# Kernel tuning notes

Measured on AMD Instinct MI355X. Metric: run time of the kernel, lower is better.

## Reference

```python
import jax, jax.numpy as jnp
import numpy as np

N_INP = 10
N_REC = 200
ALPHA = 0.1          # dt / tau = 0.01 / 0.1
NOISE_STD = 0.01
W_REC_SCALE = 0.5
W_INP_SCALE = 0.1
BATCH = 256
T = 1000


def setup_inputs() -> dict:
    key = jax.random.key(0)
    kx, kwi, kwr = jax.random.split(key, 3)
    x = jax.random.normal(kx, (BATCH, T, N_INP), dtype=jnp.float32)
    h0 = jnp.zeros((BATCH, N_REC), dtype=jnp.float32)
    W_inp = (W_INP_SCALE / np.sqrt(N_INP)) * jax.random.normal(kwi, (N_REC, N_INP), dtype=jnp.float32)
    W_rec = (W_REC_SCALE / np.sqrt(N_REC)) * jax.random.normal(kwr, (N_REC, N_REC), dtype=jnp.float32)
    b_rec = jnp.zeros((N_REC,), dtype=jnp.float32)
    return {"x": x, "h0": h0, "W_inp": W_inp, "W_rec": W_rec, "b_rec": b_rec}


def reference(x, h0, W_inp, W_rec, b_rec):
    """Euler-discretized rate RNN: h' = h + alpha*(-h + tanh(W_rec h + W_inp x + b) + noise).
    Returns states: [batch, time, n_rec]."""
    B, Tlen, _ = x.shape
    # Precompute input drive for all timesteps in one GEMM: [B,T,n_rec]
    inp_term = jnp.einsum('bti,ri->btr', x, W_inp) + b_rec
    # Per-step noise, deterministic key (mirrors torch.randn_like each step)
    noise_key = jax.random.key(42)
    eta = NOISE_STD * jax.random.normal(noise_key, (Tlen, B, W_rec.shape[0]), dtype=x.dtype)

    def step(h, xs):
        inp_t, eta_t = xs
        preact = h @ W_rec.T + inp_t          # [B, n_rec]
        rate = jnp.tanh(preact)
        h_next = h + ALPHA * (-h + rate + eta_t)
        return h_next, h_next

    _, states = jax.lax.scan(step, h0, (jnp.swapaxes(inp_term, 0, 1), eta))
    return jnp.swapaxes(states, 0, 1)  # [B, T, n_rec]
```

## Files before the change

kernel.cpp:

```cpp
#include <hip/hip_runtime.h>
#include <cstdint>
#include <cstddef>

#define TSTEPS 1000
#define NB     256
#define NR     200
#define NI     10
#define ALPHA_F     0.1f
#define NOISE_STD_F 0.01f
#define ETA_STRIDE  (NB * NR)
#define ETA_FLOATS  ((size_t)TSTEPS * NB * NR)

__device__ __forceinline__ uint32_t rotl32(uint32_t v, uint32_t d) {
  return (v << d) | (v >> (32u - d));
}

__device__ __forceinline__ uint32_t threefry_bits(uint32_t c1) {
  const uint32_t ks0 = 0u;
  const uint32_t ks1 = 42u;
  const uint32_t ks2 = 0x1BD11BDAu ^ ks0 ^ ks1;
  uint32_t x0 = ks0;
  uint32_t x1 = c1 + ks1;
#define TFR(r) { x0 += x1; x1 = rotl32(x1, (r)); x1 ^= x0; }
  TFR(13) TFR(15) TFR(26) TFR(6)   x0 += ks1; x1 += ks2 + 1u;
// ... 40 lines not shown
  const float lo = -0.99999994f;
  float u = fmaf(f, 2.0f, lo);
  u = fmaxf(lo, u);
  return 1.41421356f * erfinv_f32(u);
}

__device__ __forceinline__ float tanh_fast(float y) {
  float ay = fabsf(y);
  float t  = __expf(-2.0f * ay);
  float r  = (1.0f - t) * __frcp_rn(1.0f + t);
  return copysignf(r, y);
}

__device__ __forceinline__ void wg_barrier_lds() {
  asm volatile("s_waitcnt lgkmcnt(0)\n\ts_barrier" ::: "memory");
}

__launch_bounds__(256)
__global__ void noise_fill(float* __restrict__ ws) {
  const int64_t nq = (int64_t)ETA_FLOATS / 4;
  const int64_t stride = (int64_t)gridDim.x * blockDim.x;
  for (int64_t i = (int64_t)blockIdx.x * blockDim.x + threadIdx.x;
       i < nq; i += stride) {
    uint32_t base = (uint32_t)(i * 4);
    float4 v;
    v.x = NOISE_STD_F * jax_normal(base + 0u);
    v.y = NOISE_STD_F * jax_normal(base + 1u);
    v.z = NOISE_STD_F * jax_normal(base + 2u);
    v.w = NOISE_STD_F * jax_normal(base + 3u);
    ((float4*)ws)[i] = v;
  }
}

template <int CUR, bool PF, bool PRE>
__device__ __forceinline__ void rnn_step(
    int t, int tid, bool mac_active,
    const float (&w)[4][20], const float (&winp)[NI], float brec_r,
    float& h_reg, float*& obp, float& xnA, float& xnB,
    float4& enA, float4& enB,
    const float* __restrict__ xb, const float* __restrict__ etab,
    uint32_t nb_b,
    const float* __restrict__ hp, float* __restrict__ part_wp,
    float* __restrict__ sh_h, float* __restrict__ sh_part,
    float (*__restrict__ sh_x)[16], float (*__restrict__ sh_eta)[NR]) {
  constexpr int NXT = CUR ^ 1;

  if (mac_active) {
    float a0 = 0.0f, a1 = 0.0f, a2 = 0.0f, a3 = 0.0f;
#pragma unroll
    for (int q = 0; q < 5; ++q) {
      float4 hv = *(const float4*)(hp + 4 * q);
      a0 = fmaf(w[0][4 * q + 0], hv.x, a0);
      a1 = fmaf(w[1][4 * q + 0], hv.x, a1);
      a2 = fmaf(w[2][4 * q + 0], hv.x, a2);
      a3 = fmaf(w[3][4 * q + 0], hv.x, a3);
      a0 = fmaf(w[0][4 * q + 1], hv.y, a0);
      a1 = fmaf(w[1][4 * q + 1], hv.y, a1);
      a2 = fmaf(w[2][4 * q + 1], hv.y, a2);
      a3 = fmaf(w[3][4 * q + 1], hv.y, a3);
      a0 = fmaf(w[0][4 * q + 2], hv.z, a0);
      a1 = fmaf(w[1][4 * q + 2], hv.z, a1);
      a2 = fmaf(w[2][4 * q + 2], hv.z, a2);
      a3 = fmaf(w[3][4 * q + 2], hv.z, a3);
      a0 = fmaf(w[0][4 * q + 3], hv.w, a0);
      a1 = fmaf(w[1][4 * q + 3], hv.w, a1);
      a2 = fmaf(w[2][4 * q + 3], hv.w, a2);
      a3 = fmaf(w[3][4 * q + 3], hv.w, a3);
    }
    *(float4*)part_wp = make_float4(a0, a1, a2, a3);
  }
  wg_barrier_lds();

  if (tid < NR) {
    float y = brec_r;
#pragma unroll
    for (int q = 0; q < 10; ++q) y += sh_part[q * NR + tid];
    float4 xv0 = *(const float4*)(&sh_x[CUR][0]);
    float4 xv1 = *(const float4*)(&sh_x[CUR][4]);
    float2 xv2 = *(const float2*)(&sh_x[CUR][8]);
    y = fmaf(winp[0], xv0.x, y);
    y = fmaf(winp[1], xv0.y, y);
    y = fmaf(winp[2], xv0.z, y);
    y = fmaf(winp[3], xv0.w, y);
    y = fmaf(winp[4], xv1.x, y);
    y = fmaf(winp[5], xv1.y, y);
    y = fmaf(winp[6], xv1.z, y);
    y = fmaf(winp[7], xv1.w, y);
    y = fmaf(winp[8], xv2.x, y);
    y = fmaf(winp[9], xv2.y, y);
    float rate = tanh_fast(y);
    float eta  = sh_eta[CUR][tid];
    float hn = h_reg + ALPHA_F * (((-h_reg) + rate) + eta);
    h_reg = hn;
    sh_h[tid] = hn;
    *obp = hn;
    obp += NR;
  } else if (PRE ? (tid >= 256 && tid < 256 + NR / 4)
                 : ((tid >= 256 && tid < 448) || (tid < 208))) {
    if (PF) {
      if constexpr (PRE) {
        int j = tid - 256;
        *(float4*)(&sh_eta[NXT][4 * j]) = (CUR == 0) ? enA : enB;
        int tf = t + 3;
        if (tf > TSTEPS - 1) tf = TSTEPS - 1;
        float4 e = *(const float4*)(etab + (size_t)tf * ETA_STRIDE + 4 * j);
        if (CUR == 0) enA = e; else enB = e;
      } else {
        int n = (tid >= 256) ? (tid - 256) : (tid - 8);
        uint32_t idx = (uint32_t)(t + 1) * (uint32_t)(NB * NR) + nb_b + (uint32_t)n;
        sh_eta[NXT][n] = NOISE_STD_F * jax_normal(idx);
      }
    }
  } else if (tid >= 448 && tid < 448 + NI) {
    if (PF) {
      int j = tid - 448;
      sh_x[NXT][j] = (CUR == 0) ? xnA : xnB;
      int tf = t + 3;
      if (tf > TSTEPS - 1) tf = TSTEPS - 1;
      float xl = xb[tf * NI + j];
      if (CUR == 0) xnA = xl; else xnB = xl;
    }
  }
  wg_barrier_lds();
}

template <bool PRE>
__global__ __launch_bounds__(512, 2)
void rnn_persistent(const float* __restrict__ x,
                    const float* __restrict__ h0,
                    const float* __restrict__ Winp,
                    const float* __restrict__ Wrec,
                    const float* __restrict__ brec,
                    const float* __restrict__ eta_ws,
                    float* __restrict__ out) {
  const int b   = blockIdx.x;
  const int tid = threadIdx.x;

  __shared__ float sh_h[NR];
  __shared__ float sh_part[10 * NR];
  __shared__ float sh_x[2][16];
  __shared__ float sh_eta[2][NR];

  const int  k_th = tid / 50;
  const int  r_th = tid % 50;
  const bool mac_active = (tid < 500);

  float w[4][20];
  if (mac_active) {
#pragma unroll
    for (int j = 0; j < 4; ++j) {
      const float* wr = Wrec + (size_t)(4 * r_th + j) * NR + 20 * k_th;
#pragma unroll
      for (int q = 0; q < 5; ++q) {
        float4 v = *(const float4*)(wr + 4 * q);
        w[j][4 * q + 0] = v.x; w[j][4 * q + 1] = v.y;
        w[j][4 * q + 2] = v.z; w[j][4 * q + 3] = v.w;
      }
    }
  }

  float winp[NI];
  float brec_r = 0.0f;
  float h_reg  = 0.0f;
  float* obp   = nullptr;

  const float* xb   = x + (size_t)b * TSTEPS * NI;
  const float* etab = PRE ? (eta_ws + (size_t)b * NR) : nullptr;
  float* ob         = out + (size_t)b * TSTEPS * NR;

  if (tid < NR) {
#pragma unroll
    for (int i = 0; i < NI; ++i) winp[i] = Winp[tid * NI + i];
    brec_r = brec[tid];
    h_reg  = h0[(size_t)b * NR + tid];
    sh_h[tid] = h_reg;
    obp = ob + tid;
  }

  const uint32_t nb_b = (uint32_t)b * (uint32_t)NR;
  float  xnA = 0.0f, xnB = 0.0f;
  float4 enA = make_float4(0.f, 0.f, 0.f, 0.f);
  float4 enB = make_float4(0.f, 0.f, 0.f, 0.f);

  if constexpr (PRE) {
    if (tid >= 256 && tid < 256 + NR / 4) {
      int j = tid - 256;
      *(float4*)(&sh_eta[0][4 * j]) = *(const float4*)(etab + 4 * j);
      enA = *(const float4*)(etab + (size_t)1 * ETA_STRIDE + 4 * j);
      enB = *(const float4*)(etab + (size_t)2 * ETA_STRIDE + 4 * j);
    }
  } else {
    if ((tid >= 256 && tid < 448) || (tid >= 200 && tid < 208)) {
      int n = (tid >= 256) ? (tid - 256) : (tid - 8);
      sh_eta[0][n] = NOISE_STD_F * jax_normal(nb_b + (uint32_t)n);
    }
  }
  if (tid >= 448 && tid < 448 + NI) {
    int j = tid - 448;
    sh_x[0][j] = xb[j];
    xnA = xb[NI + j];
    xnB = xb[2 * NI + j];
  }
  __syncthreads();

  const float* hp      = sh_h + 20 * k_th;
  float*       part_wp = sh_part + k_th * NR + 4 * r_th;

  for (int t = 0; t < TSTEPS - 2; t += 2) {
    rnn_step<0, true, PRE>(t,     tid, mac_active, w, winp, brec_r, h_reg, obp,
                           xnA, xnB, enA, enB, xb, etab, nb_b, hp, part_wp,
                           sh_h, sh_part, sh_x, sh_eta);
    rnn_step<1, true, PRE>(t + 1, tid, mac_active, w, winp, brec_r, h_reg, obp,
                           xnA, xnB, enA, enB, xb, etab, nb_b, hp, part_wp,
                           sh_h, sh_part, sh_x, sh_eta);
  }
  rnn_step<0, true,  PRE>(TSTEPS - 2, tid, mac_active, w, winp, brec_r, h_reg, obp,
                          xnA, xnB, enA, enB, xb, etab, nb_b, hp, part_wp,
                          sh_h, sh_part, sh_x, sh_eta);
  rnn_step<1, false, PRE>(TSTEPS - 1, tid, mac_active, w, winp, brec_r, h_reg, obp,
                          xnA, xnB, enA, enB, xb, etab, nb_b, hp, part_wp,
                          sh_h, sh_part, sh_x, sh_eta);
}

extern "C" void kernel_launch(void* const* d_in, const int* in_sizes, int n_in,
                              void* d_out, int out_size, void* d_ws, size_t ws_size,
                              hipStream_t stream) {
  const float* x    = (const float*)d_in[0];
  const float* h0   = (const float*)d_in[1];
  const float* Winp = (const float*)d_in[2];
  const float* Wrec = (const float*)d_in[3];
  const float* brec = (const float*)d_in[4];
  float* out = (float*)d_out;
  (void)in_sizes; (void)n_in; (void)out_size;

  const size_t eta_bytes = ETA_FLOATS * sizeof(float);
  if (d_ws != nullptr && ws_size >= eta_bytes) {
    noise_fill<<<dim3(4096), dim3(256), 0, stream>>>((float*)d_ws);
    rnn_persistent<true><<<dim3(NB), dim3(512), 0, stream>>>(
        x, h0, Winp, Wrec, brec, (const float*)d_ws, out);
  } else {
    rnn_persistent<false><<<dim3(NB), dim3(512), 0, stream>>>(
        x, h0, Winp, Wrec, brec, nullptr, out);
  }
}
```

Before: 885.7 us.

## Pack two batch rows per workgroup and ping-pong matvec with update phases

```diff
diff --git a/kernel.cpp b/kernel.cpp
--- a/kernel.cpp
+++ b/kernel.cpp
@@ -96,20 +96,13 @@
   }
 }
 
-template <int CUR, bool PF, bool PRE>
-__device__ __forceinline__ void rnn_step(
-    int t, int tid, bool mac_active,
-    const float (&w)[4][20], const float (&winp)[NI], float brec_r,
-    float& h_reg, float*& obp, float& xnA, float& xnB,
-    float4& enA, float4& enB,
-    const float* __restrict__ xb, const float* __restrict__ etab,
-    uint32_t nb_b,
-    const float* __restrict__ hp, float* __restrict__ part_wp,
-    float* __restrict__ sh_h, float* __restrict__ sh_part,
-    float (*__restrict__ sh_x)[16], float (*__restrict__ sh_eta)[NR]) {
-  constexpr int NXT = CUR ^ 1;
-
-  if (mac_active) {
+
+__device__ __forceinline__ void do_mac(
+    bool mac_active, const float (&w)[4][40],
+    const float* __restrict__ hp,
+    float* __restrict__ p0, float* __restrict__ p1) {
+  if (!mac_active) return;
+  {
     float a0 = 0.0f, a1 = 0.0f, a2 = 0.0f, a3 = 0.0f;
 #pragma unroll
     for (int q = 0; q < 5; ++q) {
@@ -131,10 +124,236 @@
       a2 = fmaf(w[2][4 * q + 3], hv.w, a2);
       a3 = fmaf(w[3][4 * q + 3], hv.w, a3);
     }
+    *(float4*)p0 = make_float4(a0, a1, a2, a3);
+  }
+  {
+    float a0 = 0.0f, a1 = 0.0f, a2 = 0.0f, a3 = 0.0f;
+#pragma unroll
+    for (int q = 0; q < 5; ++q) {
+      float4 hv = *(const float4*)(hp + 20 + 4 * q);
+      a0 = fmaf(w[0][20 + 4 * q + 0], hv.x, a0);
+      a1 = fmaf(w[1][20 + 4 * q + 0], hv.x, a1);
+      a2 = fmaf(w[2][20 + 4 * q + 0], hv.x, a2);
+      a3 = fmaf(w[3][20 + 4 * q + 0], hv.x, a3);
+      a0 = fmaf(w[0][20 + 4 * q + 1], hv.y, a0);
+      a1 = fmaf(w[1][20 + 4 * q + 1], hv.y, a1);
+      a2 = fmaf(w[2][20 + 4 * q + 1], hv.y, a2);
+      a3 = fmaf(w[3][20 + 4 * q + 1], hv.y, a3);
+      a0 = fmaf(w[0][20 + 4 * q + 2], hv.z, a0);
+      a1 = fmaf(w[1][20 + 4 * q + 2], hv.z, a1);
+      a2 = fmaf(w[2][20 + 4 * q + 2], hv.z, a2);
+      a3 = fmaf(w[3][20 + 4 * q + 2], hv.z, a3);
+      a0 = fmaf(w[0][20 + 4 * q + 3], hv.w, a0);
+      a1 = fmaf(w[1][20 + 4 * q + 3], hv.w, a1);
+      a2 = fmaf(w[2][20 + 4 * q + 3], hv.w, a2);
+      a3 = fmaf(w[3][20 + 4 * q + 3], hv.w, a3);
+    }
+    *(float4*)p1 = make_float4(a0, a1, a2, a3);
+  }
+}
+
+template <int CUR, bool PF>
+__device__ __forceinline__ void do_upd(
+    int t, int lt,
+    const float (&winp)[NI], float brec_r, float& h_reg, float*& obp,
+    float4& enA, float4& enB, float2& xnA, float2& xnB,
+    const float* __restrict__ xb, const float* __restrict__ etab,
+    float* __restrict__ g_h, const float* __restrict__ g_part,
+    float (*__restrict__ g_x)[16], float (*__restrict__ g_eta)[NR]) {
+  constexpr int NXT = CUR ^ 1;
+  if (lt < NR) {
+    float y = brec_r;
+#pragma unroll
+    for (int q = 0; q < 10; ++q) y += g_part[q * NR + lt];
+    float4 xv0 = *(const float4*)(&g_x[CUR][0]);
+    float4 xv1 = *(const float4*)(&g_x[CUR][4]);
+    float2 xv2 = *(const float2*)(&g_x[CUR][8]);
+    y = fmaf(winp[0], xv0.x, y);
+    y = fmaf(winp[1], xv0.y, y);
+    y = fmaf(winp[2], xv0.z, y);
+    y = fmaf(winp[3], xv0.w, y);
+    y = fmaf(winp[4], xv1.x, y);
+    y = fmaf(winp[5], xv1.y, y);
+    y = fmaf(winp[6], xv1.z, y);
+    y = fmaf(winp[7], xv1.w, y);
+    y = fmaf(winp[8], xv2.x, y);
+    y = fmaf(winp[9], xv2.y, y);
+    float rate = tanh_fast(y);
+    float eta  = g_eta[CUR][lt];
+    float hn = h_reg + ALPHA_F * (((-h_reg) + rate) + eta);
+    h_reg = hn;
+    g_h[lt] = hn;
+    *obp = hn;
+    obp += NR;
+  } else if (lt < 250) {
+    if (PF) {
+      int j = lt - 200;
+      *(float4*)(&g_eta[NXT][4 * j]) = (CUR == 0) ? enA : enB;
+      int tf = t + 3;
+      if (tf > TSTEPS - 1) tf = TSTEPS - 1;
+      float4 e = *(const float4*)(etab + (size_t)tf * ETA_STRIDE + 4 * j);
+      if (CUR == 0) enA = e; else enB = e;
+    }
+  } else if (lt < 255) {
+    if (PF) {
+      int j = lt - 250;
+      *(float2*)(&g_x[NXT][2 * j]) = (CUR == 0) ? xnA : xnB;
+      int tf = t + 3;
+      if (tf > TSTEPS - 1) tf = TSTEPS - 1;
+      float2 xl = *(const float2*)(xb + tf * NI + 2 * j);
+      if (CUR == 0) xnA = xl; else xnB = xl;
+    }
+  }
+}
+
+__launch_bounds__(512, 2)
+__global__ void rnn_dual(const float* __restrict__ x,
+                         const float* __restrict__ h0,
+                         const float* __restrict__ Winp,
+                         const float* __restrict__ Wrec,
+                         const float* __restrict__ brec,
+                         const float* __restrict__ eta_ws,
+                         float* __restrict__ out) {
+  const int wg  = blockIdx.x;
+  const int tid = threadIdx.x;
+  const int grp = tid >> 8;
+  const int lt  = tid & 255;
+  const int b   = 2 * wg + grp;
+
+  __shared__ float sh_h[2][NR];
+  __shared__ float sh_part[2][10 * NR];
+  __shared__ float sh_x[2][2][16];
+  __shared__ float sh_eta[2][2][NR];
+
+  float* g_h    = sh_h[grp];
+  float* g_part = sh_part[grp];
+  float (*g_x)[16]  = sh_x[grp];
+  float (*g_eta)[NR] = sh_eta[grp];
+
+  const int  k_th = lt / 50;
+  const int  r_th = lt % 50;
+  const bool mac_active = (lt < 250);
+
+  float w[4][40];
+  if (mac_active) {
+#pragma unroll
+    for (int j = 0; j < 4; ++j) {
+      const float* wr = Wrec + (size_t)(4 * r_th + j) * NR + 40 * k_th;
+#pragma unroll
+      for (int q = 0; q < 10; ++q) {
+        float4 v = *(const float4*)(wr + 4 * q);
+        w[j][4 * q + 0] = v.x; w[j][4 * q + 1] = v.y;
+        w[j][4 * q + 2] = v.z; w[j][4 * q + 3] = v.w;
+      }
+    }
+  }
+
+  float winp[NI];
+  float brec_r = 0.0f;
+  float h_reg  = 0.0f;
+  float* obp   = nullptr;
+
+  const float* xb   = x + (size_t)b * TSTEPS * NI;
+  const float* etab = eta_ws + (size_t)b * NR;
+  float* ob         = out + (size_t)b * TSTEPS * NR;
+
+  if (lt < NR) {
+#pragma unroll
+    for (int i = 0; i < NI; ++i) winp[i] = Winp[lt * NI + i];
+    brec_r = brec[lt];
+    h_reg  = h0[(size_t)b * NR + lt];
+    g_h[lt] = h_reg;
+    obp = ob + lt;
+  }
+
+  float4 enA = make_float4(0.f, 0.f, 0.f, 0.f);
+  float4 enB = make_float4(0.f, 0.f, 0.f, 0.f);
+  float2 xnA = make_float2(0.f, 0.f);
+  float2 xnB = make_float2(0.f, 0.f);
+
+  if (lt >= 200 && lt < 250) {
+    int j = lt - 200;
+    *(float4*)(&g_eta[0][4 * j]) = *(const float4*)(etab + 4 * j);
+    enA = *(const float4*)(etab + (size_t)1 * ETA_STRIDE + 4 * j);
+    enB = *(const float4*)(etab + (size_t)2 * ETA_STRIDE + 4 * j);
+  } else if (lt >= 250 && lt < 255) {
+    int j = lt - 250;
+    *(float2*)(&g_x[0][2 * j]) = *(const float2*)(xb + 2 * j);
+    xnA = *(const float2*)(xb + NI + 2 * j);
+    xnB = *(const float2*)(xb + 2 * NI + 2 * j);
+  }
+  __syncthreads();
+
+  const float* hp = g_h + 40 * k_th;
+  float* p0 = g_part + (size_t)(2 * k_th) * NR + 4 * r_th;
+  float* p1 = g_part + (size_t)(2 * k_th + 1) * NR + 4 * r_th;
+
+  if (grp == 0) do_mac(mac_active, w, hp, p0, p1);
+  wg_barrier_lds();
+
+#define SLOT_B(I, C, P)                                                     \
+  if (grp == 0) do_upd<C, P>((I), lt, winp, brec_r, h_reg, obp, enA, enB,   \
+                             xnA, xnB, xb, etab, g_h, g_part, g_x, g_eta);  \
+  else          do_mac(mac_active, w, hp, p0, p1);                          \
+  wg_barrier_lds();
+#define SLOT_A(I, C, P)                                                     \
+  if (grp == 0) do_mac(mac_active, w, hp, p0, p1);                          \
+  else          do_upd<C, P>((I)-1, lt, winp, brec_r, h_reg, obp, enA, enB, \
+                             xnA, xnB, xb, etab, g_h, g_part, g_x, g_eta);  \
+  wg_barrier_lds();
+
+  for (int i = 0; i < TSTEPS - 2; i += 2) {
+    SLOT_B(i,     0, true)
+    SLOT_A(i + 1, 0, true)
+    SLOT_B(i + 1, 1, true)
+    SLOT_A(i + 2, 1, true)
+  }
+  SLOT_B(TSTEPS - 2, 0, true)
+  SLOT_A(TSTEPS - 1, 0, true)
+  SLOT_B(TSTEPS - 1, 1, false)
+  if (grp == 1) {
+    do_upd<1, false>(TSTEPS - 1, lt, winp, brec_r, h_reg, obp, enA, enB,
+                     xnA, xnB, xb, etab, g_h, g_part, g_x, g_eta);
+  }
+#undef SLOT_A
+#undef SLOT_B
+}
+
+template <int CUR, bool PF>
+__device__ __forceinline__ void fb_step(
+    int t, int tid, bool mac_active,
+    const float (&w)[4][20], const float (&winp)[NI], float brec_r,
+    float& h_reg, float*& obp, float& xnA, float& xnB,
+    const float* __restrict__ xb, uint32_t nb_b,
+    const float* __restrict__ hp, float* __restrict__ part_wp,
+    float* __restrict__ sh_h, float* __restrict__ sh_part,
+    float (*__restrict__ sh_x)[16], float (*__restrict__ sh_eta)[NR]) {
+  constexpr int NXT = CUR ^ 1;
+  if (mac_active) {
+    float a0 = 0.0f, a1 = 0.0f, a2 = 0.0f, a3 = 0.0f;
+#pragma unroll
+    for (int q = 0; q < 5; ++q) {
+      float4 hv = *(const float4*)(hp + 4 * q);
+      a0 = fmaf(w[0][4 * q + 0], hv.x, a0);
+      a1 = fmaf(w[1][4 * q + 0], hv.x, a1);
+      a2 = fmaf(w[2][4 * q + 0], hv.x, a2);
+      a3 = fmaf(w[3][4 * q + 0], hv.x, a3);
+      a0 = fmaf(w[0][4 * q + 1], hv.y, a0);
+      a1 = fmaf(w[1][4 * q + 1], hv.y, a1);
+      a2 = fmaf(w[2][4 * q + 1], hv.y, a2);
+      a3 = fmaf(w[3][4 * q + 1], hv.y, a3);
+      a0 = fmaf(w[0][4 * q + 2], hv.z, a0);
+      a1 = fmaf(w[1][4 * q + 2], hv.z, a1);
+      a2 = fmaf(w[2][4 * q + 2], hv.z, a2);
+      a3 = fmaf(w[3][4 * q + 2], hv.z, a3);
+      a0 = fmaf(w[0][4 * q + 3], hv.w, a0);
+      a1 = fmaf(w[1][4 * q + 3], hv.w, a1);
+      a2 = fmaf(w[2][4 * q + 3], hv.w, a2);
+      a3 = fmaf(w[3][4 * q + 3], hv.w, a3);
+    }
     *(float4*)part_wp = make_float4(a0, a1, a2, a3);
   }
   wg_barrier_lds();
-
   if (tid < NR) {
     float y = brec_r;
 #pragma unroll
@@ -159,21 +378,11 @@
     sh_h[tid] = hn;
     *obp = hn;
     obp += NR;
-  } else if (PRE ? (tid >= 256 && tid < 256 + NR / 4)
-                 : ((tid >= 256 && tid < 448) || (tid < 208))) {
+  } else if ((tid >= 256 && tid < 448) || (tid < 208)) {
     if (PF) {
-      if constexpr (PRE) {
-        int j = tid - 256;
-        *(float4*)(&sh_eta[NXT][4 * j]) = (CUR == 0) ? enA : enB;
-        int tf = t + 3;
-        if (tf > TSTEPS - 1) tf = TSTEPS - 1;
-        float4 e = *(const float4*)(etab + (size_t)tf * ETA_STRIDE + 4 * j);
-        if (CUR == 0) enA = e; else enB = e;
-      } else {
-        int n = (tid >= 256) ? (tid - 256) : (tid - 8);
-        uint32_t idx = (uint32_t)(t + 1) * (uint32_t)(NB * NR) + nb_b + (uint32_t)n;
-        sh_eta[NXT][n] = NOISE_STD_F * jax_normal(idx);
-      }
+      int n = (tid >= 256) ? (tid - 256) : (tid - 8);
+      uint32_t idx = (uint32_t)(t + 1) * (uint32_t)(NB * NR) + nb_b + (uint32_t)n;
+      sh_eta[NXT][n] = NOISE_STD_F * jax_normal(idx);
     }
   } else if (tid >= 448 && tid < 448 + NI) {
     if (PF) {
@@ -188,27 +397,22 @@
   wg_barrier_lds();
 }
 
-template <bool PRE>
 __global__ __launch_bounds__(512, 2)
-void rnn_persistent(const float* __restrict__ x,
-                    const float* __restrict__ h0,
-                    const float* __restrict__ Winp,
-                    const float* __restrict__ Wrec,
-                    const float* __restrict__ brec,
-                    const float* __restrict__ eta_ws,
-                    float* __restrict__ out) {
+void rnn_fallback(const float* __restrict__ x,
+                  const float* __restrict__ h0,
+                  const float* __restrict__ Winp,
+                  const float* __restrict__ Wrec,
+                  const float* __restrict__ brec,
+                  float* __restrict__ out) {
   const int b   = blockIdx.x;
   const int tid = threadIdx.x;
-
   __shared__ float sh_h[NR];
   __shared__ float sh_part[10 * NR];
   __shared__ float sh_x[2][16];
   __shared__ float sh_eta[2][NR];
-
   const int  k_th = tid / 50;
   const int  r_th = tid % 50;
   const bool mac_active = (tid < 500);
-
   float w[4][20];
   if (mac_active) {
 #pragma unroll
@@ -222,16 +426,11 @@
       }
     }
   }
-
   float winp[NI];
-  float brec_r = 0.0f;
-  float h_reg  = 0.0f;
-  float* obp   = nullptr;
-
-  const float* xb   = x + (size_t)b * TSTEPS * NI;
-  const float* etab = PRE ? (eta_ws + (size_t)b * NR) : nullptr;
-  float* ob         = out + (size_t)b * TSTEPS * NR;
-
+  float brec_r = 0.0f, h_reg = 0.0f;
+  float* obp = nullptr;
+  const float* xb = x + (size_t)b * TSTEPS * NI;
+  float* ob       = out + (size_t)b * TSTEPS * NR;
   if (tid < NR) {
 #pragma unroll
     for (int i = 0; i < NI; ++i) winp[i] = Winp[tid * NI + i];
@@ -240,24 +439,11 @@
     sh_h[tid] = h_reg;
     obp = ob + tid;
   }
-
   const uint32_t nb_b = (uint32_t)b * (uint32_t)NR;
-  float  xnA = 0.0f, xnB = 0.0f;
-  float4 enA = make_float4(0.f, 0.f, 0.f, 0.f);
-  float4 enB = make_float4(0.f, 0.f, 0.f, 0.f);
-
-  if constexpr (PRE) {
-    if (tid >= 256 && tid < 256 + NR / 4) {
-      int j = tid - 256;
-      *(float4*)(&sh_eta[0][4 * j]) = *(const float4*)(etab + 4 * j);
-      enA = *(const float4*)(etab + (size_t)1 * ETA_STRIDE + 4 * j);
-      enB = *(const float4*)(etab + (size_t)2 * ETA_STRIDE + 4 * j);
-    }
-  } else {
-    if ((tid >= 256 && tid < 448) || (tid >= 200 && tid < 208)) {
-      int n = (tid >= 256) ? (tid - 256) : (tid - 8);
-      sh_eta[0][n] = NOISE_STD_F * jax_normal(nb_b + (uint32_t)n);
-    }
+  float xnA = 0.0f, xnB = 0.0f;
+  if ((tid >= 256 && tid < 448) || (tid >= 200 && tid < 208)) {
+    int n = (tid >= 256) ? (tid - 256) : (tid - 8);
+    sh_eta[0][n] = NOISE_STD_F * jax_normal(nb_b + (uint32_t)n);
   }
   if (tid >= 448 && tid < 448 + NI) {
     int j = tid - 448;
@@ -266,24 +452,18 @@
     xnB = xb[2 * NI + j];
   }
   __syncthreads();
-
   const float* hp      = sh_h + 20 * k_th;
   float*       part_wp = sh_part + k_th * NR + 4 * r_th;
-
   for (int t = 0; t < TSTEPS - 2; t += 2) {
-    rnn_step<0, true, PRE>(t,     tid, mac_active, w, winp, brec_r, h_reg, obp,
-                           xnA, xnB, enA, enB, xb, etab, nb_b, hp, part_wp,
-                           sh_h, sh_part, sh_x, sh_eta);
-    rnn_step<1, true, PRE>(t + 1, tid, mac_active, w, winp, brec_r, h_reg, obp,
-                           xnA, xnB, enA, enB, xb, etab, nb_b, hp, part_wp,
-                           sh_h, sh_part, sh_x, sh_eta);
-  }
-  rnn_step<0, true,  PRE>(TSTEPS - 2, tid, mac_active, w, winp, brec_r, h_reg, obp,
-                          xnA, xnB, enA, enB, xb, etab, nb_b, hp, part_wp,
-                          sh_h, sh_part, sh_x, sh_eta);
-  rnn_step<1, false, PRE>(TSTEPS - 1, tid, mac_active, w, winp, brec_r, h_reg, obp,
-                          xnA, xnB, enA, enB, xb, etab, nb_b, hp, part_wp,
-                          sh_h, sh_part, sh_x, sh_eta);
+    fb_step<0, true>(t,     tid, mac_active, w, winp, brec_r, h_reg, obp,
+                     xnA, xnB, xb, nb_b, hp, part_wp, sh_h, sh_part, sh_x, sh_eta);
+    fb_step<1, true>(t + 1, tid, mac_active, w, winp, brec_r, h_reg, obp,
+                     xnA, xnB, xb, nb_b, hp, part_wp, sh_h, sh_part, sh_x, sh_eta);
+  }
+  fb_step<0, true >(TSTEPS - 2, tid, mac_active, w, winp, brec_r, h_reg, obp,
+                    xnA, xnB, xb, nb_b, hp, part_wp, sh_h, sh_part, sh_x, sh_eta);
+  fb_step<1, false>(TSTEPS - 1, tid, mac_active, w, winp, brec_r, h_reg, obp,
+                    xnA, xnB, xb, nb_b, hp, part_wp, sh_h, sh_part, sh_x, sh_eta);
 }
 
 extern "C" void kernel_launch(void* const* d_in, const int* in_sizes, int n_in,
@@ -300,10 +480,10 @@
   const size_t eta_bytes = ETA_FLOATS * sizeof(float);
   if (d_ws != nullptr && ws_size >= eta_bytes) {
     noise_fill<<<dim3(4096), dim3(256), 0, stream>>>((float*)d_ws);
-    rnn_persistent<true><<<dim3(NB), dim3(512), 0, stream>>>(
+    rnn_dual<<<dim3(NB / 2), dim3(512), 0, stream>>>(
         x, h0, Winp, Wrec, brec, (const float*)d_ws, out);
   } else {
-    rnn_persistent<false><<<dim3(NB), dim3(512), 0, stream>>>(
-        x, h0, Winp, Wrec, brec, nullptr, out);
-  }
-}
+    rnn_fallback<<<dim3(NB), dim3(512), 0, stream>>>(
+        x, h0, Winp, Wrec, brec, out);
+  }
+}
```

New measurement: 1.759 ms. 98.6% more time.

## Keep full W_rec rows in registers, one thread per output row

Applied to the files above, without the earlier changes.

```diff
diff --git a/kernel.cpp b/kernel.cpp
--- a/kernel.cpp
+++ b/kernel.cpp
@@ -96,19 +96,186 @@
   }
 }
 
-template <int CUR, bool PF, bool PRE>
-__device__ __forceinline__ void rnn_step(
+
+#define DECLW(q) \
+  float W_##q##_0 = 0.f, W_##q##_1 = 0.f, W_##q##_2 = 0.f, W_##q##_3 = 0.f, \
+        W_##q##_4 = 0.f, W_##q##_5 = 0.f, W_##q##_6 = 0.f, W_##q##_7 = 0.f, \
+        W_##q##_8 = 0.f, W_##q##_9 = 0.f, W_##q##_10 = 0.f, W_##q##_11 = 0.f,\
+        W_##q##_12 = 0.f, W_##q##_13 = 0.f, W_##q##_14 = 0.f,               \
+        W_##q##_15 = 0.f, W_##q##_16 = 0.f, W_##q##_17 = 0.f,               \
+        W_##q##_18 = 0.f, W_##q##_19 = 0.f;
+
+#define LOADW(q) {                                                          \
+  const float* wp_ = wr + 20 * (q);                                         \
+  float4 a_  = *(const float4*)(wp_);                                       \
+  float4 b_  = *(const float4*)(wp_ + 4);                                   \
+  float4 c_  = *(const float4*)(wp_ + 8);                                   \
+  float4 d_  = *(const float4*)(wp_ + 12);                                  \
+  float4 e4_ = *(const float4*)(wp_ + 16);                                  \
+  W_##q##_0  = a_.x;  W_##q##_1  = a_.y;  W_##q##_2  = a_.z;                \
+  W_##q##_3  = a_.w;  W_##q##_4  = b_.x;  W_##q##_5  = b_.y;                \
+  W_##q##_6  = b_.z;  W_##q##_7  = b_.w;  W_##q##_8  = c_.x;                \
+  W_##q##_9  = c_.y;  W_##q##_10 = c_.z;  W_##q##_11 = c_.w;                \
+  W_##q##_12 = d_.x;  W_##q##_13 = d_.y;  W_##q##_14 = d_.z;                \
+  W_##q##_15 = d_.w;  W_##q##_16 = e4_.x; W_##q##_17 = e4_.y;               \
+  W_##q##_18 = e4_.z; W_##q##_19 = e4_.w; }
+
+#define FMAC(q) {                                                           \
+  const float* hq_ = hb + 20 * (q);                                         \
+  float4 a_  = *(const float4*)(hq_);                                       \
+  float4 b_  = *(const float4*)(hq_ + 4);                                   \
+  float4 c_  = *(const float4*)(hq_ + 8);                                   \
+  float4 d_  = *(const float4*)(hq_ + 12);                                  \
+  float4 e4_ = *(const float4*)(hq_ + 16);                                  \
+  float p_ = 0.0f;                                                          \
+  p_ = fmaf(W_##q##_0,  a_.x,  p_);                                         \
+  p_ = fmaf(W_##q##_1,  a_.y,  p_);                                         \
+  p_ = fmaf(W_##q##_2,  a_.z,  p_);                                         \
+  p_ = fmaf(W_##q##_3,  a_.w,  p_);                                         \
+  p_ = fmaf(W_##q##_4,  b_.x,  p_);                                         \
+  p_ = fmaf(W_##q##_5,  b_.y,  p_);                                         \
+  p_ = fmaf(W_##q##_6,  b_.z,  p_);                                         \
+  p_ = fmaf(W_##q##_7,  b_.w,  p_);                                         \
+  p_ = fmaf(W_##q##_8,  c_.x,  p_);                                         \
+  p_ = fmaf(W_##q##_9,  c_.y,  p_);                                         \
+  p_ = fmaf(W_##q##_10, c_.z,  p_);                                         \
+  p_ = fmaf(W_##q##_11, c_.w,  p_);                                         \
+  p_ = fmaf(W_##q##_12, d_.x,  p_);                                         \
+  p_ = fmaf(W_##q##_13, d_.y,  p_);                                         \
+  p_ = fmaf(W_##q##_14, d_.z,  p_);                                         \
+  p_ = fmaf(W_##q##_15, d_.w,  p_);                                         \
+  p_ = fmaf(W_##q##_16, e4_.x, p_);                                         \
+  p_ = fmaf(W_##q##_17, e4_.y, p_);                                         \
+  p_ = fmaf(W_##q##_18, e4_.z, p_);                                         \
+  p_ = fmaf(W_##q##_19, e4_.w, p_);                                         \
+  y += p_; }
+
+#define STEP(CURI, TT, PF_) {                                               \
+  if (ln < 50) {                                                            \
+    const float* hb = sh_h[CURI];                                           \
+    float y = brec_r;                                                       \
+    FMAC(0) FMAC(1) FMAC(2) FMAC(3) FMAC(4)                                 \
+    FMAC(5) FMAC(6) FMAC(7) FMAC(8) FMAC(9)                                 \
+    float4 xv0 = *(const float4*)(&sh_x[CURI][0]);                          \
+    float4 xv1 = *(const float4*)(&sh_x[CURI][4]);                          \
+    float2 xv2 = *(const float2*)(&sh_x[CURI][8]);                          \
+    y = fmaf(winp0, xv0.x, y);                                              \
+    y = fmaf(winp1, xv0.y, y);                                              \
+    y = fmaf(winp2, xv0.z, y);                                              \
+    y = fmaf(winp3, xv0.w, y);                                              \
+    y = fmaf(winp4, xv1.x, y);                                              \
+    y = fmaf(winp5, xv1.y, y);                                              \
+    y = fmaf(winp6, xv1.z, y);                                              \
+    y = fmaf(winp7, xv1.w, y);                                              \
+    y = fmaf(winp8, xv2.x, y);                                              \
+    y = fmaf(winp9, xv2.y, y);                                              \
+    float rate = tanh_fast(y);                                              \
+    float eta  = sh_eta[CURI][row];                                         \
+    float hn = h_reg + ALPHA_F * (((-h_reg) + rate) + eta);                 \
+    h_reg = hn;                                                             \
+    sh_h[(CURI) ^ 1][row] = hn;                                             \
+    *obp = hn;                                                              \
+    obp += NR;                                                              \
+  } else if (elane) {                                                       \
+    if (PF_) {                                                              \
+      *(float4*)(&sh_eta[(CURI) ^ 1][4 * eidx]) =                           \
+          ((CURI) == 0) ? enA : enB;                                        \
+      int tf = (TT) + 3;                                                    \
+      if (tf > TSTEPS - 1) tf = TSTEPS - 1;                                 \
+      float4 e_ = *(const float4*)(etab + (size_t)tf * ETA_STRIDE + 4 * eidx);\
+      if ((CURI) == 0) enA = e_; else enB = e_;                             \
+    }                                                                       \
+  } else if (xlane) {                                                       \
+    if (PF_) {                                                              \
+      *(float2*)(&sh_x[(CURI) ^ 1][2 * xj]) = ((CURI) == 0) ? xnA : xnB;    \
+      int tf = (TT) + 3;                                                    \
+      if (tf > TSTEPS - 1) tf = TSTEPS - 1;                                 \
+      float2 x_ = *(const float2*)(xb + tf * NI + 2 * xj);                  \
+      if ((CURI) == 0) xnA = x_; else xnB = x_;                             \
+    }                                                                       \
+  }                                                                         \
+  wg_barrier_lds(); }
+
+__launch_bounds__(256, 1)
+__global__ void rnn_rowreg(const float* __restrict__ x,
+                           const float* __restrict__ h0,
+                           const float* __restrict__ Winp,
+                           const float* __restrict__ Wrec,
+                           const float* __restrict__ brec,
+                           const float* __restrict__ eta_ws,
+                           float* __restrict__ out) {
+  const int b   = blockIdx.x;
+  const int tid = threadIdx.x;
+  const int wv  = tid >> 6;
+  const int ln  = tid & 63;
+
+  __shared__ float sh_h[2][NR];
+  __shared__ float sh_eta[2][NR];
+  __shared__ float sh_x[2][16];
+
+  const int  row  = wv * 50 + ln;
+  const int  eidx = wv * 13 + (ln - 50);
+  const bool elane = (ln >= 50) && (ln < 63) && (eidx < 50);
+  const bool xlane = (ln == 63) || (wv == 3 && ln == 61);
+  const int  xj    = (ln == 63) ? wv : 4;
+
+  const float* xb   = x + (size_t)b * TSTEPS * NI;
+  const float* etab = eta_ws + (size_t)b * NR;
+  float* ob         = out + (size_t)b * TSTEPS * NR;
+
+  DECLW(0) DECLW(1) DECLW(2) DECLW(3) DECLW(4)
+  DECLW(5) DECLW(6) DECLW(7) DECLW(8) DECLW(9)
+  float winp0 = 0.f, winp1 = 0.f, winp2 = 0.f, winp3 = 0.f, winp4 = 0.f;
+  float winp5 = 0.f, winp6 = 0.f, winp7 = 0.f, winp8 = 0.f, winp9 = 0.f;
+  float brec_r = 0.0f;
+  float h_reg  = 0.0f;
+  float* obp   = nullptr;
+  float4 enA = make_float4(0.f, 0.f, 0.f, 0.f);
+  float4 enB = make_float4(0.f, 0.f, 0.f, 0.f);
+  float2 xnA = make_float2(0.f, 0.f);
+  float2 xnB = make_float2(0.f, 0.f);
+
+  if (ln < 50) {
+    const float* wr = Wrec + (size_t)row * NR;
+    LOADW(0) LOADW(1) LOADW(2) LOADW(3) LOADW(4)
+    LOADW(5) LOADW(6) LOADW(7) LOADW(8) LOADW(9)
+    const float* wi = Winp + (size_t)row * NI;
+    winp0 = wi[0]; winp1 = wi[1]; winp2 = wi[2]; winp3 = wi[3];
+    winp4 = wi[4]; winp5 = wi[5]; winp6 = wi[6]; winp7 = wi[7];
+    winp8 = wi[8]; winp9 = wi[9];
+    brec_r = brec[row];
+    h_reg  = h0[(size_t)b * NR + row];
+    sh_h[0][row] = h_reg;
+    obp = ob + row;
+  } else if (elane) {
+    *(float4*)(&sh_eta[0][4 * eidx]) = *(const float4*)(etab + 4 * eidx);
+    enA = *(const float4*)(etab + (size_t)1 * ETA_STRIDE + 4 * eidx);
+    enB = *(const float4*)(etab + (size_t)2 * ETA_STRIDE + 4 * eidx);
+  } else if (xlane) {
+    *(float2*)(&sh_x[0][2 * xj]) = *(const float2*)(xb + 2 * xj);
+    xnA = *(const float2*)(xb + NI + 2 * xj);
+    xnB = *(const float2*)(xb + 2 * NI + 2 * xj);
+  }
+  __syncthreads();
+
+  for (int t = 0; t < TSTEPS - 2; t += 2) {
+    STEP(0, t,     true)
+    STEP(1, t + 1, true)
+  }
+  STEP(0, TSTEPS - 2, true)
+  STEP(1, TSTEPS - 1, false)
+}
+
+template <int CUR, bool PF>
+__device__ __forceinline__ void fb_step(
     int t, int tid, bool mac_active,
     const float (&w)[4][20], const float (&winp)[NI], float brec_r,
     float& h_reg, float*& obp, float& xnA, float& xnB,
-    float4& enA, float4& enB,
-    const float* __restrict__ xb, const float* __restrict__ etab,
-    uint32_t nb_b,
+    const float* __restrict__ xb, uint32_t nb_b,
     const float* __restrict__ hp, float* __restrict__ part_wp,
     float* __restrict__ sh_h, float* __restrict__ sh_part,
     float (*__restrict__ sh_x)[16], float (*__restrict__ sh_eta)[NR]) {
   constexpr int NXT = CUR ^ 1;
-
   if (mac_active) {
     float a0 = 0.0f, a1 = 0.0f, a2 = 0.0f, a3 = 0.0f;
 #pragma unroll
@@ -134,7 +301,6 @@
     *(float4*)part_wp = make_float4(a0, a1, a2, a3);
   }
   wg_barrier_lds();
-
   if (tid < NR) {
     float y = brec_r;
 #pragma unroll
@@ -159,21 +325,11 @@
     sh_h[tid] = hn;
     *obp = hn;
     obp += NR;
-  } else if (PRE ? (tid >= 256 && tid < 256 + NR / 4)
-                 : ((tid >= 256 && tid < 448) || (tid < 208))) {
+  } else if ((tid >= 256 && tid < 448) || (tid < 208)) {
     if (PF) {
-      if constexpr (PRE) {
-        int j = tid - 256;
-        *(float4*)(&sh_eta[NXT][4 * j]) = (CUR == 0) ? enA : enB;
-        int tf = t + 3;
-        if (tf > TSTEPS - 1) tf = TSTEPS - 1;
-        float4 e = *(const float4*)(etab + (size_t)tf * ETA_STRIDE + 4 * j);
-        if (CUR == 0) enA = e; else enB = e;
-      } else {
-        int n = (tid >= 256) ? (tid - 256) : (tid - 8);
-        uint32_t idx = (uint32_t)(t + 1) * (uint32_t)(NB * NR) + nb_b + (uint32_t)n;
-        sh_eta[NXT][n] = NOISE_STD_F * jax_normal(idx);
-      }
+      int n = (tid >= 256) ? (tid - 256) : (tid - 8);
+      uint32_t idx = (uint32_t)(t + 1) * (uint32_t)(NB * NR) + nb_b + (uint32_t)n;
+      sh_eta[NXT][n] = NOISE_STD_F * jax_normal(idx);
     }
   } else if (tid >= 448 && tid < 448 + NI) {
     if (PF) {
@@ -188,27 +344,22 @@
   wg_barrier_lds();
 }
 
-template <bool PRE>
 __global__ __launch_bounds__(512, 2)
-void rnn_persistent(const float* __restrict__ x,
-                    const float* __restrict__ h0,
-                    const float* __restrict__ Winp,
-                    const float* __restrict__ Wrec,
-                    const float* __restrict__ brec,
-                    const float* __restrict__ eta_ws,
-                    float* __restrict__ out) {
+void rnn_fallback(const float* __restrict__ x,
+                  const float* __restrict__ h0,
+                  const float* __restrict__ Winp,
+                  const float* __restrict__ Wrec,
+                  const float* __restrict__ brec,
+                  float* __restrict__ out) {
   const int b   = blockIdx.x;
   const int tid = threadIdx.x;
-
   __shared__ float sh_h[NR];
   __shared__ float sh_part[10 * NR];
   __shared__ float sh_x[2][16];
   __shared__ float sh_eta[2][NR];
-
   const int  k_th = tid / 50;
   const int  r_th = tid % 50;
   const bool mac_active = (tid < 500);
-
   float w[4][20];
   if (mac_active) {
 #pragma unroll
@@ -222,16 +373,11 @@
       }
     }
   }
-
   float winp[NI];
-  float brec_r = 0.0f;
-  float h_reg  = 0.0f;
-  float* obp   = nullptr;
-
-  const float* xb   = x + (size_t)b * TSTEPS * NI;
-  const float* etab = PRE ? (eta_ws + (size_t)b * NR) : nullptr;
-  float* ob         = out + (size_t)b * TSTEPS * NR;
-
+  float brec_r = 0.0f, h_reg = 0.0f;
+  float* obp = nullptr;
+  const float* xb = x + (size_t)b * TSTEPS * NI;
+  float* ob       = out + (size_t)b * TSTEPS * NR;
   if (tid < NR) {
 #pragma unroll
     for (int i = 0; i < NI; ++i) winp[i] = Winp[tid * NI + i];
@@ -240,24 +386,11 @@
     sh_h[tid] = h_reg;
     obp = ob + tid;
   }
-
   const uint32_t nb_b = (uint32_t)b * (uint32_t)NR;
-  float  xnA = 0.0f, xnB = 0.0f;
-  float4 enA = make_float4(0.f, 0.f, 0.f, 0.f);
-  float4 enB = make_float4(0.f, 0.f, 0.f, 0.f);
-
-  if constexpr (PRE) {
-    if (tid >= 256 && tid < 256 + NR / 4) {
-      int j = tid - 256;
-      *(float4*)(&sh_eta[0][4 * j]) = *(const float4*)(etab + 4 * j);
-      enA = *(const float4*)(etab + (size_t)1 * ETA_STRIDE + 4 * j);
-      enB = *(const float4*)(etab + (size_t)2 * ETA_STRIDE + 4 * j);
-    }
-  } else {
-    if ((tid >= 256 && tid < 448) || (tid >= 200 && tid < 208)) {
-      int n = (tid >= 256) ? (tid - 256) : (tid - 8);
-      sh_eta[0][n] = NOISE_STD_F * jax_normal(nb_b + (uint32_t)n);
-    }
+  float xnA = 0.0f, xnB = 0.0f;
+  if ((tid >= 256 && tid < 448) || (tid >= 200 && tid < 208)) {
+    int n = (tid >= 256) ? (tid - 256) : (tid - 8);
+    sh_eta[0][n] = NOISE_STD_F * jax_normal(nb_b + (uint32_t)n);
   }
   if (tid >= 448 && tid < 448 + NI) {
     int j = tid - 448;
@@ -266,24 +399,18 @@
     xnB = xb[2 * NI + j];
   }
   __syncthreads();
-
   const float* hp      = sh_h + 20 * k_th;
   float*       part_wp = sh_part + k_th * NR + 4 * r_th;
-
   for (int t = 0; t < TSTEPS - 2; t += 2) {
-    rnn_step<0, true, PRE>(t,     tid, mac_active, w, winp, brec_r, h_reg, obp,
-                           xnA, xnB, enA, enB, xb, etab, nb_b, hp, part_wp,
-                           sh_h, sh_part, sh_x, sh_eta);
-    rnn_step<1, true, PRE>(t + 1, tid, mac_active, w, winp, brec_r, h_reg, obp,
-                           xnA, xnB, enA, enB, xb, etab, nb_b, hp, part_wp,
-                           sh_h, sh_part, sh_x, sh_eta);
-  }
-  rnn_step<0, true,  PRE>(TSTEPS - 2, tid, mac_active, w, winp, brec_r, h_reg, obp,
-                          xnA, xnB, enA, enB, xb, etab, nb_b, hp, part_wp,
-                          sh_h, sh_part, sh_x, sh_eta);
-  rnn_step<1, false, PRE>(TSTEPS - 1, tid, mac_active, w, winp, brec_r, h_reg, obp,
-                          xnA, xnB, enA, enB, xb, etab, nb_b, hp, part_wp,
-                          sh_h, sh_part, sh_x, sh_eta);
+    fb_step<0, true>(t,     tid, mac_active, w, winp, brec_r, h_reg, obp,
+                     xnA, xnB, xb, nb_b, hp, part_wp, sh_h, sh_part, sh_x, sh_eta);
+    fb_step<1, true>(t + 1, tid, mac_active, w, winp, brec_r, h_reg, obp,
+                     xnA, xnB, xb, nb_b, hp, part_wp, sh_h, sh_part, sh_x, sh_eta);
+  }
+  fb_step<0, true >(TSTEPS - 2, tid, mac_active, w, winp, brec_r, h_reg, obp,
+                    xnA, xnB, xb, nb_b, hp, part_wp, sh_h, sh_part, sh_x, sh_eta);
+  fb_step<1, false>(TSTEPS - 1, tid, mac_active, w, winp, brec_r, h_reg, obp,
+                    xnA, xnB, xb, nb_b, hp, part_wp, sh_h, sh_part, sh_x, sh_eta);
 }
 
 extern "C" void kernel_launch(void* const* d_in, const int* in_sizes, int n_in,
@@ -300,10 +427,10 @@
   const size_t eta_bytes = ETA_FLOATS * sizeof(float);
   if (d_ws != nullptr && ws_size >= eta_bytes) {
     noise_fill<<<dim3(4096), dim3(256), 0, stream>>>((float*)d_ws);
-    rnn_persistent<true><<<dim3(NB), dim3(512), 0, stream>>>(
+    rnn_rowreg<<<dim3(NB), dim3(256), 0, stream>>>(
         x, h0, Winp, Wrec, brec, (const float*)d_ws, out);
   } else {
-    rnn_persistent<false><<<dim3(NB), dim3(512), 0, stream>>>(
-        x, h0, Winp, Wrec, brec, nullptr, out);
-  }
-}
+    rnn_fallback<<<dim3(NB), dim3(512), 0, stream>>>(
+        x, h0, Winp, Wrec, brec, out);
+  }
+}
```

New measurement: 1.421 ms. +60.5%, slower.

## Restructure RNN step into 8-row MAC tiles with separate update waves

Applied to the files above, without the earlier changes.

```diff
diff --git a/kernel.cpp b/kernel.cpp
--- a/kernel.cpp
+++ b/kernel.cpp
@@ -96,19 +96,184 @@
   }
 }
 
-template <int CUR, bool PF, bool PRE>
-__device__ __forceinline__ void rnn_step(
+
+#define DECLW8(r) float4 W##r##_0, W##r##_1, W##r##_2, W##r##_3, W##r##_4;
+
+#define LOADW8(r) {                                                         \
+  const float* wp_ = Wrec + (size_t)(8 * r_th + (r)) * NR + 20 * k_th;      \
+  W##r##_0 = *(const float4*)(wp_);                                         \
+  W##r##_1 = *(const float4*)(wp_ + 4);                                     \
+  W##r##_2 = *(const float4*)(wp_ + 8);                                     \
+  W##r##_3 = *(const float4*)(wp_ + 12);                                    \
+  W##r##_4 = *(const float4*)(wp_ + 16); }
+
+#define ROWACC(r)                                                           \
+  float a##r = 0.0f;                                                        \
+  a##r = fmaf(W##r##_0.x, h0_.x, a##r);                                     \
+  a##r = fmaf(W##r##_0.y, h0_.y, a##r);                                     \
+  a##r = fmaf(W##r##_0.z, h0_.z, a##r);                                     \
+  a##r = fmaf(W##r##_0.w, h0_.w, a##r);                                     \
+  a##r = fmaf(W##r##_1.x, h1_.x, a##r);                                     \
+  a##r = fmaf(W##r##_1.y, h1_.y, a##r);                                     \
+  a##r = fmaf(W##r##_1.z, h1_.z, a##r);                                     \
+  a##r = fmaf(W##r##_1.w, h1_.w, a##r);                                     \
+  a##r = fmaf(W##r##_2.x, h2_.x, a##r);                                     \
+  a##r = fmaf(W##r##_2.y, h2_.y, a##r);                                     \
+  a##r = fmaf(W##r##_2.z, h2_.z, a##r);                                     \
+  a##r = fmaf(W##r##_2.w, h2_.w, a##r);                                     \
+  a##r = fmaf(W##r##_3.x, h3_.x, a##r);                                     \
+  a##r = fmaf(W##r##_3.y, h3_.y, a##r);                                     \
+  a##r = fmaf(W##r##_3.z, h3_.z, a##r);                                     \
+  a##r = fmaf(W##r##_3.w, h3_.w, a##r);                                     \
+  a##r = fmaf(W##r##_4.x, h4_.x, a##r);                                     \
+  a##r = fmaf(W##r##_4.y, h4_.y, a##r);                                     \
+  a##r = fmaf(W##r##_4.z, h4_.z, a##r);                                     \
+  a##r = fmaf(W##r##_4.w, h4_.w, a##r);
+
+#define STEP(CURI, TT) {                                                    \
+                        \
+  if (mac_active) {                                                         \
+    float4 h0_ = *(const float4*)(hb);                                      \
+    float4 h1_ = *(const float4*)(hb + 4);                                  \
+    float4 h2_ = *(const float4*)(hb + 8);                                  \
+    float4 h3_ = *(const float4*)(hb + 12);                                 \
+    float4 h4_ = *(const float4*)(hb + 16);                                 \
+    ROWACC(0) ROWACC(1) ROWACC(2) ROWACC(3)                                 \
+    ROWACC(4) ROWACC(5) ROWACC(6) ROWACC(7)                                 \
+    *(float4*)pw0 = make_float4(a0, a1, a2, a3);                            \
+    *(float4*)pw1 = make_float4(a4, a5, a6, a7);                            \
+  }                                                                         \
+  wg_barrier_lds();                                                         \
+                        \
+  if (upd_active) {                                                         \
+    float y = brec_r;                                                       \
+    y += pr[0 * 208];                                                       \
+    y += pr[1 * 208];                                                       \
+    y += pr[2 * 208];                                                       \
+    y += pr[3 * 208];                                                       \
+    y += pr[4 * 208];                                                       \
+    y += pr[5 * 208];                                                       \
+    y += pr[6 * 208];                                                       \
+    y += pr[7 * 208];                                                       \
+    y += pr[8 * 208];                                                       \
+    y += pr[9 * 208];                                                       \
+    float4 xv0 = *(const float4*)(&sh_x[CURI][0]);                          \
+    float4 xv1 = *(const float4*)(&sh_x[CURI][4]);                          \
+    float2 xv2 = *(const float2*)(&sh_x[CURI][8]);                          \
+    y = fmaf(winp[0], xv0.x, y);                                            \
+    y = fmaf(winp[1], xv0.y, y);                                            \
+    y = fmaf(winp[2], xv0.z, y);                                            \
+    y = fmaf(winp[3], xv0.w, y);                                            \
+    y = fmaf(winp[4], xv1.x, y);                                            \
+    y = fmaf(winp[5], xv1.y, y);                                            \
+    y = fmaf(winp[6], xv1.z, y);                                            \
+    y = fmaf(winp[7], xv1.w, y);                                            \
+    y = fmaf(winp[8], xv2.x, y);                                            \
+    y = fmaf(winp[9], xv2.y, y);                                            \
+    float rate = tanh_fast(y);                                              \
+    float eta  = (CURI == 0) ? etaA : etaB;                                 \
+    float hn = h_reg + ALPHA_F * (((-h_reg) + rate) + eta);                 \
+    h_reg = hn;                                                             \
+    sh_h[urow] = hn;                                                        \
+    *obp = hn;                                                              \
+    obp += NR;                                                              \
+    int tf_ = (TT) + 2;                                                     \
+    if (tf_ > TSTEPS - 1) tf_ = TSTEPS - 1;    \
+    float e_ = etab[(size_t)tf_ * ETA_STRIDE + urow];                       \
+    if (CURI == 0) etaA = e_; else etaB = e_;                               \
+  } else if (xpipe) {                                                       \
+    *(float2*)(&sh_x[(CURI) ^ 1][2 * xj]) = (CURI == 0) ? xnA : xnB;        \
+    int tf_ = (TT) + 3;                                                     \
+    if (tf_ > TSTEPS - 1) tf_ = TSTEPS - 1;                                 \
+    float2 x_ = *(const float2*)(xb + tf_ * NI + 2 * xj);                   \
+    if (CURI == 0) xnA = x_; else xnB = x_;                                 \
+  }                                                                         \
+  wg_barrier_lds(); }
+
+__launch_bounds__(512, 1)
+__global__ void rnn_r8(const float* __restrict__ x,
+                       const float* __restrict__ h0,
+                       const float* __restrict__ Winp,
+                       const float* __restrict__ Wrec,
+                       const float* __restrict__ brec,
+                       const float* __restrict__ eta_ws,
+                       float* __restrict__ out) {
+  const int b   = blockIdx.x;
+  const int tid = threadIdx.x;
+  const int wv  = tid >> 6;
+  const int ln  = tid & 63;
+
+  __shared__ float sh_h[NR];
+  __shared__ float sh_part[10 * 208];
+  __shared__ float sh_x[2][16];
+
+  const bool mac_active = (tid < 250);
+  const int  k_th = tid / 25;
+  const int  r_th = tid % 25;
+
+  const bool upd_active = (wv >= 4) && (ln < 50);
+  const int  urow = (wv - 4) * 50 + ln;
+  const bool xpipe = (wv == 4) && (ln >= 50) && (ln < 55);
+  const int  xj    = ln - 50;
+
+  const float* xb   = x + (size_t)b * TSTEPS * NI;
+  const float* etab = eta_ws + (size_t)b * NR;
+  float* ob         = out + (size_t)b * TSTEPS * NR;
+
+  DECLW8(0) DECLW8(1) DECLW8(2) DECLW8(3)
+  DECLW8(4) DECLW8(5) DECLW8(6) DECLW8(7)
+  const float* hb = nullptr;
+  float* pw0 = nullptr;
+  float* pw1 = nullptr;
+
+  float winp[NI];
+  float brec_r = 0.0f;
+  float h_reg  = 0.0f;
+  float etaA = 0.0f, etaB = 0.0f;
+  float* obp = nullptr;
+  const float* pr = nullptr;
+  float2 xnA = make_float2(0.f, 0.f);
+  float2 xnB = make_float2(0.f, 0.f);
+
+  if (mac_active) {
+    LOADW8(0) LOADW8(1) LOADW8(2) LOADW8(3)
+    LOADW8(4) LOADW8(5) LOADW8(6) LOADW8(7)
+    hb  = sh_h + 20 * k_th;
+    pw0 = sh_part + 208 * k_th + 4 * r_th;
+    pw1 = pw0 + 104;
+  } else if (upd_active) {
+#pragma unroll
+    for (int i = 0; i < NI; ++i) winp[i] = Winp[urow * NI + i];
+    brec_r = brec[urow];
+    h_reg  = h0[(size_t)b * NR + urow];
+    sh_h[urow] = h_reg;
+    obp = ob + urow;
+    pr = sh_part + 4 * (urow >> 3) + (urow & 3) + ((urow & 7) >= 4 ? 104 : 0);
+    etaA = etab[urow];
+    etaB = etab[(size_t)1 * ETA_STRIDE + urow];
+  } else if (xpipe) {
+    *(float2*)(&sh_x[0][2 * xj]) = *(const float2*)(xb + 2 * xj);
+    xnA = *(const float2*)(xb + NI + 2 * xj);
+    xnB = *(const float2*)(xb + 2 * NI + 2 * xj);
+  }
+  __syncthreads();
+
+  for (int t = 0; t < TSTEPS; t += 2) {
+    STEP(0, t)
+    STEP(1, t + 1)
+  }
+}
+
+template <int CUR, bool PF>
+__device__ __forceinline__ void fb_step(
     int t, int tid, bool mac_active,
     const float (&w)[4][20], const float (&winp)[NI], float brec_r,
     float& h_reg, float*& obp, float& xnA, float& xnB,
-    float4& enA, float4& enB,
-    const float* __restrict__ xb, const float* __restrict__ etab,
-    uint32_t nb_b,
+    const float* __restrict__ xb, uint32_t nb_b,
     const float* __restrict__ hp, float* __restrict__ part_wp,
     float* __restrict__ sh_h, float* __restrict__ sh_part,
     float (*__restrict__ sh_x)[16], float (*__restrict__ sh_eta)[NR]) {
   constexpr int NXT = CUR ^ 1;
-
   if (mac_active) {
     float a0 = 0.0f, a1 = 0.0f, a2 = 0.0f, a3 = 0.0f;
 #pragma unroll
@@ -134,7 +299,6 @@
     *(float4*)part_wp = make_float4(a0, a1, a2, a3);
   }
   wg_barrier_lds();
-
   if (tid < NR) {
     float y = brec_r;
 #pragma unroll
@@ -159,21 +323,11 @@
     sh_h[tid] = hn;
     *obp = hn;
     obp += NR;
-  } else if (PRE ? (tid >= 256 && tid < 256 + NR / 4)
-                 : ((tid >= 256 && tid < 448) || (tid < 208))) {
+  } else if ((tid >= 256 && tid < 448) || (tid < 208)) {
     if (PF) {
-      if constexpr (PRE) {
-        int j = tid - 256;
-        *(float4*)(&sh_eta[NXT][4 * j]) = (CUR == 0) ? enA : enB;
-        int tf = t + 3;
-        if (tf > TSTEPS - 1) tf = TSTEPS - 1;
-        float4 e = *(const float4*)(etab + (size_t)tf * ETA_STRIDE + 4 * j);
-        if (CUR == 0) enA = e; else enB = e;
-      } else {
-        int n = (tid >= 256) ? (tid - 256) : (tid - 8);
-        uint32_t idx = (uint32_t)(t + 1) * (uint32_t)(NB * NR) + nb_b + (uint32_t)n;
-        sh_eta[NXT][n] = NOISE_STD_F * jax_normal(idx);
-      }
+      int n = (tid >= 256) ? (tid - 256) : (tid - 8);
+      uint32_t idx = (uint32_t)(t + 1) * (uint32_t)(NB * NR) + nb_b + (uint32_t)n;
+      sh_eta[NXT][n] = NOISE_STD_F * jax_normal(idx);
     }
   } else if (tid >= 448 && tid < 448 + NI) {
     if (PF) {
@@ -188,27 +342,22 @@
   wg_barrier_lds();
 }
 
-template <bool PRE>
 __global__ __launch_bounds__(512, 2)
-void rnn_persistent(const float* __restrict__ x,
-                    const float* __restrict__ h0,
-                    const float* __restrict__ Winp,
-                    const float* __restrict__ Wrec,
-                    const float* __restrict__ brec,
-                    const float* __restrict__ eta_ws,
-                    float* __restrict__ out) {
+void rnn_fallback(const float* __restrict__ x,
+                  const float* __restrict__ h0,
+                  const float* __restrict__ Winp,
+                  const float* __restrict__ Wrec,
+                  const float* __restrict__ brec,
+                  float* __restrict__ out) {
   const int b   = blockIdx.x;
   const int tid = threadIdx.x;
-
   __shared__ float sh_h[NR];
   __shared__ float sh_part[10 * NR];
   __shared__ float sh_x[2][16];
   __shared__ float sh_eta[2][NR];
-
   const int  k_th = tid / 50;
   const int  r_th = tid % 50;
   const bool mac_active = (tid < 500);
-
   float w[4][20];
   if (mac_active) {
 #pragma unroll
@@ -222,16 +371,11 @@
       }
     }
   }
-
   float winp[NI];
-  float brec_r = 0.0f;
-  float h_reg  = 0.0f;
-  float* obp   = nullptr;
-
-  const float* xb   = x + (size_t)b * TSTEPS * NI;
-  const float* etab = PRE ? (eta_ws + (size_t)b * NR) : nullptr;
-  float* ob         = out + (size_t)b * TSTEPS * NR;
-
+  float brec_r = 0.0f, h_reg = 0.0f;
+  float* obp = nullptr;
+  const float* xb = x + (size_t)b * TSTEPS * NI;
+  float* ob       = out + (size_t)b * TSTEPS * NR;
   if (tid < NR) {
 #pragma unroll
     for (int i = 0; i < NI; ++i) winp[i] = Winp[tid * NI + i];
@@ -240,24 +384,11 @@
     sh_h[tid] = h_reg;
     obp = ob + tid;
   }
-
   const uint32_t nb_b = (uint32_t)b * (uint32_t)NR;
-  float  xnA = 0.0f, xnB = 0.0f;
-  float4 enA = make_float4(0.f, 0.f, 0.f, 0.f);
-  float4 enB = make_float4(0.f, 0.f, 0.f, 0.f);
-
-  if constexpr (PRE) {
-    if (tid >= 256 && tid < 256 + NR / 4) {
-      int j = tid - 256;
-      *(float4*)(&sh_eta[0][4 * j]) = *(const float4*)(etab + 4 * j);
-      enA = *(const float4*)(etab + (size_t)1 * ETA_STRIDE + 4 * j);
-      enB = *(const float4*)(etab + (size_t)2 * ETA_STRIDE + 4 * j);
-    }
-  } else {
-    if ((tid >= 256 && tid < 448) || (tid >= 200 && tid < 208)) {
-      int n = (tid >= 256) ? (tid - 256) : (tid - 8);
-      sh_eta[0][n] = NOISE_STD_F * jax_normal(nb_b + (uint32_t)n);
-    }
+  float xnA = 0.0f, xnB = 0.0f;
+  if ((tid >= 256 && tid < 448) || (tid >= 200 && tid < 208)) {
+    int n = (tid >= 256) ? (tid - 256) : (tid - 8);
+    sh_eta[0][n] = NOISE_STD_F * jax_normal(nb_b + (uint32_t)n);
   }
   if (tid >= 448 && tid < 448 + NI) {
     int j = tid - 448;
@@ -266,24 +397,18 @@
     xnB = xb[2 * NI + j];
   }
   __syncthreads();
-
   const float* hp      = sh_h + 20 * k_th;
   float*       part_wp = sh_part + k_th * NR + 4 * r_th;
-
   for (int t = 0; t < TSTEPS - 2; t += 2) {
-    rnn_step<0, true, PRE>(t,     tid, mac_active, w, winp, brec_r, h_reg, obp,
-                           xnA, xnB, enA, enB, xb, etab, nb_b, hp, part_wp,
-                           sh_h, sh_part, sh_x, sh_eta);
-    rnn_step<1, true, PRE>(t + 1, tid, mac_active, w, winp, brec_r, h_reg, obp,
-                           xnA, xnB, enA, enB, xb, etab, nb_b, hp, part_wp,
-                           sh_h, sh_part, sh_x, sh_eta);
-  }
-  rnn_step<0, true,  PRE>(TSTEPS - 2, tid, mac_active, w, winp, brec_r, h_reg, obp,
-                          xnA, xnB, enA, enB, xb, etab, nb_b, hp, part_wp,
-                          sh_h, sh_part, sh_x, sh_eta);
-  rnn_step<1, false, PRE>(TSTEPS - 1, tid, mac_active, w, winp, brec_r, h_reg, obp,
-                          xnA, xnB, enA, enB, xb, etab, nb_b, hp, part_wp,
-                          sh_h, sh_part, sh_x, sh_eta);
+    fb_step<0, true>(t,     tid, mac_active, w, winp, brec_r, h_reg, obp,
+                     xnA, xnB, xb, nb_b, hp, part_wp, sh_h, sh_part, sh_x, sh_eta);
+    fb_step<1, true>(t + 1, tid, mac_active, w, winp, brec_r, h_reg, obp,
+                     xnA, xnB, xb, nb_b, hp, part_wp, sh_h, sh_part, sh_x, sh_eta);
+  }
+  fb_step<0, true >(TSTEPS - 2, tid, mac_active, w, winp, brec_r, h_reg, obp,
+                    xnA, xnB, xb, nb_b, hp, part_wp, sh_h, sh_part, sh_x, sh_eta);
+  fb_step<1, false>(TSTEPS - 1, tid, mac_active, w, winp, brec_r, h_reg, obp,
+                    xnA, xnB, xb, nb_b, hp, part_wp, sh_h, sh_part, sh_x, sh_eta);
 }
 
 extern "C" void kernel_launch(void* const* d_in, const int* in_sizes, int n_in,
@@ -300,10 +425,10 @@
   const size_t eta_bytes = ETA_FLOATS * sizeof(float);
   if (d_ws != nullptr && ws_size >= eta_bytes) {
     noise_fill<<<dim3(4096), dim3(256), 0, stream>>>((float*)d_ws);
-    rnn_persistent<true><<<dim3(NB), dim3(512), 0, stream>>>(
+    rnn_r8<<<dim3(NB), dim3(512), 0, stream>>>(
         x, h0, Winp, Wrec, brec, (const float*)d_ws, out);
   } else {
-    rnn_persistent<false><<<dim3(NB), dim3(512), 0, stream>>>(
-        x, h0, Winp, Wrec, brec, nullptr, out);
-  }
-}
+    rnn_fallback<<<dim3(NB), dim3(512), 0, stream>>>(
+        x, h0, Winp, Wrec, brec, out);
+  }
+}
```

New measurement: 1.010 ms. +14.1%, slower.
